# Kernel optimization log

Hardware: AMD Instinct MI355X
Metric: run time of the kernel (lower is better)

Reference implementation:

```python
import jax, jax.numpy as jnp
from jax import lax
import numpy as np

DT = 0.02
STEP_JITTER = 0.01
NUM_STEPS = 180
B, H, W, D = 2, 512, 512, 128


def setup_inputs() -> dict:
    key = jax.random.key(0)
    k1, k2, k3 = jax.random.split(key, 3)
    camera_rotation = jnp.tile(jnp.eye(3, dtype=jnp.float32)[None], (B, 1, 1))
    camera_position = jnp.array([[0.0, 0.0, -2.5], [0.3, 0.2, -2.5]], dtype=jnp.float32)
    focal = 300.0 * jnp.ones((B, 2), dtype=jnp.float32)
    principal_point = jnp.full((B, 2), 256.0, dtype=jnp.float32)
    xs = jnp.arange(W, dtype=jnp.float32)
    ys = jnp.arange(H, dtype=jnp.float32)
    gx, gy = jnp.meshgrid(xs, ys, indexing='xy')  # [H,W]
    pixel_coords = jnp.broadcast_to(jnp.stack([gx, gy], -1)[None], (B, H, W, 2))
    template = jax.random.uniform(k1, (B, 4, D, D, D), dtype=jnp.float32)  # RGB + alpha volume
    background = jax.random.uniform(k2, (B, 3, H, W), dtype=jnp.float32)
    return {
        'camera_rotation': camera_rotation, 'camera_position': camera_position,
        'focal': focal, 'principal_point': principal_point,
        'pixel_coords': pixel_coords, 'template': template, 'background': background,
    }


def _trilinear_one(vol, pos):
    # vol [C,D,D,D] indexed [c,z,y,x]; pos [H,W,3] = (x,y,z) in [-1,1]
    Dv = vol.shape[-1]
    g = jnp.clip((pos + 1.0) * 0.5 * (Dv - 1), 0.0, Dv - 1)
    gx, gy, gz = g[..., 0], g[..., 1], g[..., 2]
    x0 = jnp.floor(gx).astype(jnp.int32); x1 = jnp.minimum(x0 + 1, Dv - 1)
    y0 = jnp.floor(gy).astype(jnp.int32); y1 = jnp.minimum(y0 + 1, Dv - 1)
    z0 = jnp.floor(gz).astype(jnp.int32); z1 = jnp.minimum(z0 + 1, Dv - 1)
    wx = (gx - x0)[None]; wy = (gy - y0)[None]; wz = (gz - z0)[None]
    at = lambda z, y, x: vol[:, z, y, x]  # [C,H,W]
    c00 = at(z0, y0, x0) * (1 - wx) + at(z0, y0, x1) * wx
    c01 = at(z0, y1, x0) * (1 - wx) + at(z0, y1, x1) * wx
    c10 = at(z1, y0, x0) * (1 - wx) + at(z1, y0, x1) * wx
    c11 = at(z1, y1, x0) * (1 - wx) + at(z1, y1, x1) * wx
    c0 = c00 * (1 - wy) + c01 * wy
    c1 = c10 * (1 - wy) + c11 * wy
    return c0 * (1 - wz) + c1 * wz  # [C,H,W]


def _march(camera_rotation, camera_position, focal, principal_point, pixel_coords, template, background):
    key = jax.random.key(42)
    rd = (pixel_coords - principal_point[:, None, None, :]) / focal[:, None, None, :]
    rd = jnp.concatenate([rd, jnp.ones_like(rd[..., :1])], axis=-1)
    # torch: sum(R[:,None,None,:,:] * d[...,:,None], dim=-2) == R^T @ d
    rd = jnp.einsum('bjk,bhwj->bhwk', camera_rotation, rd)
    rd = rd / jnp.sqrt(jnp.sum(rd * rd, axis=-1, keepdims=True))
    cp = camera_position[:, None, None, :]
    # ray/box intersection (no_grad in original)
    t1 = (-1.0 - cp) / rd
    t2 = (1.0 - cp) / rd
    t_min = jnp.maximum(jnp.minimum(t1[..., 0], t2[..., 0]),
                        jnp.maximum(jnp.minimum(t1[..., 1], t2[..., 1]),
                                    jnp.minimum(t1[..., 2], t2[..., 2])))
    t_max = jnp.minimum(jnp.maximum(t1[..., 0], t2[..., 0]),
                        jnp.minimum(jnp.maximum(t1[..., 1], t2[..., 1]),
                                    jnp.maximum(t1[..., 2], t2[..., 2])))
    hit = t_min < t_max
    t = jnp.maximum(jnp.where(hit, t_min, 0.0), 0.0)
    t = lax.stop_gradient(t)
    t = t - DT * jax.random.uniform(jax.random.fold_in(key, 0), t.shape, dtype=t.dtype)
    ray_pos = cp + rd * t[..., None]                      # [B,H,W,3]
    ray_rgb = jnp.zeros_like(jnp.moveaxis(ray_pos, -1, 1))  # [B,3,H,W]
    ray_alpha = jnp.zeros_like(ray_rgb[:, :1])             # [B,1,H,W]
    ray_length = jnp.zeros_like(ray_alpha)
    sample = jax.vmap(_trilinear_one)

    def body(carry, i):
        ray_pos, t, ray_rgb, ray_alpha, ray_length = carry
        valid = jnp.all((ray_pos > -1.0) & (ray_pos < 1.0), axis=-1)
        valid_f = valid[:, None].astype(ray_rgb.dtype)      # [B,1,H,W]
        s = sample(template, ray_pos)                       # [B,4,H,W]
        sample_rgb, sample_alpha = s[:, :3], s[:, 3:4]
        noise = jax.random.normal(jax.random.fold_in(key, i + 1), t.shape, dtype=t.dtype)
        step = lax.stop_gradient(DT * jnp.exp(STEP_JITTER * noise))  # [B,H,W]
        contrib = (jnp.minimum(ray_alpha + sample_alpha * step[:, None], 1.0) - ray_alpha) * valid_f
        ray_rgb = ray_rgb + sample_rgb * contrib
        ray_alpha = ray_alpha + contrib
        ray_length = ray_length + step[:, None] * (contrib == 0)
        ray_pos = ray_pos + rd * step[..., None]
        t = t + step
        return (ray_pos, t, ray_rgb, ray_alpha, ray_length), None

    carry = (ray_pos, t, ray_rgb, ray_alpha, ray_length)
    (ray_pos, t, ray_rgb, ray_alpha, ray_length), _ = lax.scan(body, carry, jnp.arange(NUM_STEPS))
    ray_length = ray_alpha * ray_length / (jnp.max(ray_length) + jnp.min(ray_length))
    ray_rgb = ray_rgb + (1.0 - ray_alpha) * jnp.maximum(background, 0.0)
    return ray_rgb, ray_alpha, ray_length


def reference(camera_rotation, camera_position, focal, principal_point, pixel_coords, template, background):
    return _march(camera_rotation, camera_position, focal, principal_point, pixel_coords, template, background)
```

## Files before the change

### kernel.cpp

```cpp
#include <hip/hip_runtime.h>
#include <stdint.h>

#pragma clang fp contract(off)

#define Bn 2
#define Hn 512
#define Wn 512
#define Dn 128
#define HW (Hn * Wn)
#define NRAY (Bn * HW)
#define NSTEP 180
#define DTC 0.02f
#define D3 (Dn * Dn * Dn)

#define WS_AOS_BYTE_OFF 4096
#define WS_AOS_BYTES ((size_t)Bn * D3 * 16)

typedef float f2 __attribute__((ext_vector_type(2)));

#define KEXP  ((float)(0.01 * (double)1.41421354f * 1.4426950408889634))
#define LOG2DT (-5.643856189774724f)

__device__ __forceinline__ uint32_t rotl32(uint32_t x, int n) {
    return (x << n) | (x >> (32 - n));
}

__device__ __forceinline__ void tf2x32(uint32_t k0, uint32_t k1,
                                       uint32_t& x0, uint32_t& x1) {
    uint32_t k2 = k0 ^ k1 ^ 0x1BD11BDAu;
    x0 += k0; x1 += k1;
    x0 += x1; x1 = rotl32(x1, 13); x1 ^= x0;
    x0 += x1; x1 = rotl32(x1, 15); x1 ^= x0;
    x0 += x1; x1 = rotl32(x1, 26); x1 ^= x0;
    x0 += x1; x1 = rotl32(x1, 6);  x1 ^= x0;
    x0 += k1; x1 += k2 + 1u;
    x0 += x1; x1 = rotl32(x1, 17); x1 ^= x0;
    x0 += x1; x1 = rotl32(x1, 29); x1 ^= x0;
    x0 += x1; x1 = rotl32(x1, 16); x1 ^= x0;
    x0 += x1; x1 = rotl32(x1, 24); x1 ^= x0;
    x0 += k2; x1 += k0 + 2u;
    x0 += x1; x1 = rotl32(x1, 13); x1 ^= x0;
    x0 += x1; x1 = rotl32(x1, 15); x1 ^= x0;
    x0 += x1; x1 = rotl32(x1, 26); x1 ^= x0;
    x0 += x1; x1 = rotl32(x1, 6);  x1 ^= x0;
    x0 += k0; x1 += k1 + 3u;
    x0 += x1; x1 = rotl32(x1, 17); x1 ^= x0;
    x0 += x1; x1 = rotl32(x1, 29); x1 ^= x0;
    x0 += x1; x1 = rotl32(x1, 16); x1 ^= x0;
    x0 += x1; x1 = rotl32(x1, 24); x1 ^= x0;
    x0 += k1; x1 += k2 + 4u;
    x0 += x1; x1 = rotl32(x1, 13); x1 ^= x0;
    x0 += x1; x1 = rotl32(x1, 15); x1 ^= x0;
    x0 += x1; x1 = rotl32(x1, 26); x1 ^= x0;
    x0 += x1; x1 = rotl32(x1, 6);  x1 ^= x0;
    x0 += k2; x1 += k0 + 5u;
}

__device__ __forceinline__ uint32_t pbits(uint32_t k0, uint32_t k1, uint32_t i) {
    uint32_t x0 = 0u, x1 = i;
    tf2x32(k0, k1, x0, x1);
    return x0 ^ x1;
}

__device__ __forceinline__ float erfinv_px(float x) {
    float a = x * x;
    float w = -__logf(1.0f - a);
    float p;
    if (w < 5.0f) {
        w = w - 2.5f;
        p = 2.81022636e-08f;
        p = fmaf(p, w, 3.43273939e-07f);
        p = fmaf(p, w, -3.5233877e-06f);
        p = fmaf(p, w, -4.39150654e-06f);
        p = fmaf(p, w, 0.00021858087f);
        p = fmaf(p, w, -0.00125372503f);
        p = fmaf(p, w, -0.00417768164f);
        p = fmaf(p, w, 0.246640727f);
        p = fmaf(p, w, 1.50140941f);
    } else {
        w = sqrtf(w) - 3.0f;
        p = -0.000200214257f;
        p = fmaf(p, w, 0.000100950558f);
        p = fmaf(p, w, 0.00134934322f);
        p = fmaf(p, w, -0.00367342844f);
        p = fmaf(p, w, 0.00573950773f);
        p = fmaf(p, w, -0.0076224613f);
        p = fmaf(p, w, 0.00943887047f);
        p = fmaf(p, w, 1.00167406f);
        p = fmaf(p, w, 2.83297682f);
    }
    return p * x;
}

__device__ __forceinline__ float step_from_bits(uint32_t bits) {
    float uf = __uint_as_float((bits >> 9) | 0x3f800000u);
    float uu = fmaxf(-0.99999994f, fmaf(uf, 2.0f, -3.0f));
    float pw = erfinv_px(uu);
    return __builtin_amdgcn_exp2f(fmaf(pw, KEXP, LOG2DT));
}

__device__ __forceinline__ f2 plerp(f2 a, f2 b, f2 wv) {
    return __builtin_elementwise_fma(wv, b - a, a);
}

__global__ void init_keys_kernel(uint32_t* __restrict__ ws) {
    int t = threadIdx.x;
    if (t <= 180) {
        uint32_t x0 = 0u, x1 = (uint32_t)t;
        tf2x32(0u, 42u, x0, x1);
        ws[2 * t]     = x0;
        ws[2 * t + 1] = x1;
    }
    if (t == 181) ws[362] = 0u;
    if (t == 182) ws[363] = 0x7f7fffffu;
}

__global__ __launch_bounds__(256) void repack_kernel(
    const float* __restrict__ tpl, float4* __restrict__ aos,
    uint32_t* __restrict__ ws) {
    if (blockIdx.x == 0) {
        int t = threadIdx.x;
        if (t <= 180) {
            uint32_t x0 = 0u, x1 = (uint32_t)t;
            tf2x32(0u, 42u, x0, x1);
            ws[2 * t]     = x0;
            ws[2 * t + 1] = x1;
        }
        if (t == 181) ws[362] = 0u;
        if (t == 182) ws[363] = 0x7f7fffffu;
    }
    int i = blockIdx.x * 256 + threadIdx.x;
    if (i >= Bn * D3) return;
    int b = i >> 21;
    int v = i & (D3 - 1);
    const float* base = tpl + (size_t)b * 4 * D3 + v;
    float4 o;
    o.x = base[0];
    o.y = base[D3];
    o.z = base[2 * D3];
    o.w = base[3 * D3];
    aos[i] = o;
}

template <bool PACKED>
__global__ __launch_bounds__(256) void march_kernel(
    const float* __restrict__ rot, const float* __restrict__ cpos,
    const float* __restrict__ focal, const float* __restrict__ pp,
    const float* __restrict__ pix, const float* __restrict__ tpl,
    const float4* __restrict__ aos,
    const float* __restrict__ bg, float* __restrict__ out,
    uint32_t* __restrict__ ws)
{
    #pragma clang fp contract(off)
    __shared__ uint2 skeys[181];
    for (int i = threadIdx.x; i < 181; i += 256) {
        skeys[i] = make_uint2(ws[2 * i], ws[2 * i + 1]);
    }
    __syncthreads();

    const int idx = blockIdx.x * 256 + threadIdx.x;
    const int b = idx >> 18;
    const int p = idx & (HW - 1);

    float px = pix[(size_t)idx * 2 + 0];
    float py = pix[(size_t)idx * 2 + 1];
    float v0 = (px - pp[b * 2 + 0]) / focal[b * 2 + 0];
    float v1 = (py - pp[b * 2 + 1]) / focal[b * 2 + 1];
    const float* R = rot + b * 9;
    float rdx = (R[0] * v0 + R[3] * v1) + R[6];
    float rdy = (R[1] * v0 + R[4] * v1) + R[7];
    float rdz = (R[2] * v0 + R[5] * v1) + R[8];
    float nrm = sqrtf((rdx * rdx + rdy * rdy) + rdz * rdz);
    rdx = rdx / nrm; rdy = rdy / nrm; rdz = rdz / nrm;
    float cpx = cpos[b * 3 + 0], cpy = cpos[b * 3 + 1], cpz = cpos[b * 3 + 2];

    float t1x = (-1.0f - cpx) / rdx, t2x = (1.0f - cpx) / rdx;
    float t1y = (-1.0f - cpy) / rdy, t2y = (1.0f - cpy) / rdy;
    float t1z = (-1.0f - cpz) / rdz, t2z = (1.0f - cpz) / rdz;
    float tmin = fmaxf(fminf(t1x, t2x), fmaxf(fminf(t1y, t2y), fminf(t1z, t2z)));
    float tmax = fminf(fmaxf(t1x, t2x), fminf(fmaxf(t1y, t2y), fmaxf(t1z, t2z)));
    bool hit = tmin < tmax;
    float t = fmaxf(hit ? tmin : 0.0f, 0.0f);

    {
        uint2 k0 = skeys[0];
        uint32_t bits = pbits(k0.x, k0.y, (uint32_t)idx);
        float u = __uint_as_float((bits >> 9) | 0x3f800000u) - 1.0f;
        u = fmaxf(0.0f, u);
        t = t - DTC * u;
    }

    float posx = cpx + rdx * t;
    float posy = cpy + rdy * t;
    float posz = cpz + rdz * t;

    float alpha = 0.0f, len = 0.0f;
    f2 acc_rg = {0.0f, 0.0f};
    float acc_b = 0.0f;
    const float* vol = tpl + (size_t)b * 4 * D3;
    const char* vbase = (const char*)(aos + (size_t)b * D3);
    bool entered = false;

    int i = 0;
    for (; i < NSTEP; ++i) {
        uint2 kk = skeys[i + 1];
        float step = step_from_bits(pbits(kk.x, kk.y, (uint32_t)idx));

        float m = fmaxf(fmaxf(fabsf(posx), fabsf(posy)), fabsf(posz));
        bool valid = m < 1.0f;
        bool sampling = fmaxf(m, alpha) < 1.0f;

        float contrib = 0.0f;
        if (sampling) {
            float gx = fmaf(posx, 63.5f, 63.5f);
            float gy = fmaf(posy, 63.5f, 63.5f);
            float gz = fmaf(posz, 63.5f, 63.5f);
            float fx = floorf(gx), fy = floorf(gy), fz = floorf(gz);
            float wx = gx - fx, wy = gy - fy, wz = gz - fz;
            int ix0 = (int)fx, iy0 = (int)fy, iz0 = (int)fz;

            float sx, sy, sz, sw;
            if (PACKED) {
                uint32_t xb  = (uint32_t)min(ix0, Dn - 2) << 4;
                float wxe = (ix0 < Dn - 1) ? wx : 1.0f;
                uint32_t yb0 = (uint32_t)iy0 << 11;
                uint32_t yb1 = min(yb0 + (1u << 11), (uint32_t)(Dn - 1) << 11);
                uint32_t zb0 = (uint32_t)iz0 << 18;
                uint32_t zb1 = min(zb0 + (1u << 18), (uint32_t)(Dn - 1) << 18);

                uint32_t o00 = zb0 + yb0 + xb;
                uint32_t o01 = zb0 + yb1 + xb;
                uint32_t o10 = zb1 + yb0 + xb;
                uint32_t o11 = zb1 + yb1 + xb;

                float4 A00 = *(const float4*)(vbase + o00);
                float4 B00 = *(const float4*)(vbase + o00 + 16);
                float4 A01 = *(const float4*)(vbase + o01);
                float4 B01 = *(const float4*)(vbase + o01 + 16);
                float4 A10 = *(const float4*)(vbase + o10);
                float4 B10 = *(const float4*)(vbase + o10 + 16);
                float4 A11 = *(const float4*)(vbase + o11);
                float4 B11 = *(const float4*)(vbase + o11 + 16);

                f2 wxv = {wxe, wxe}, wyv = {wy, wy}, wzv = {wz, wz};
                f2 c00rg = plerp((f2){A00.x, A00.y}, (f2){B00.x, B00.y}, wxv);
                f2 c00ba = plerp((f2){A00.z, A00.w}, (f2){B00.z, B00.w}, wxv);
                f2 c01rg = plerp((f2){A01.x, A01.y}, (f2){B01.x, B01.y}, wxv);
                f2 c01ba = plerp((f2){A01.z, A01.w}, (f2){B01.z, B01.w}, wxv);
                f2 c10rg = plerp((f2){A10.x, A10.y}, (f2){B10.x, B10.y}, wxv);
                f2 c10ba = plerp((f2){A10.z, A10.w}, (f2){B10.z, B10.w}, wxv);
                f2 c11rg = plerp((f2){A11.x, A11.y}, (f2){B11.x, B11.y}, wxv);
                f2 c11ba = plerp((f2){A11.z, A11.w}, (f2){B11.z, B11.w}, wxv);
                f2 c0rg = plerp(c00rg, c01rg, wyv);
                f2 c0ba = plerp(c00ba, c01ba, wyv);
                f2 c1rg = plerp(c10rg, c11rg, wyv);
                f2 c1ba = plerp(c10ba, c11ba, wyv);
                f2 srg = plerp(c0rg, c1rg, wzv);
                f2 sba = plerp(c0ba, c1ba, wzv);
                sx = srg.x; sy = srg.y; sz = sba.x; sw = sba.y;
            } else {
                int ix1 = min(ix0 + 1, Dn - 1);
                int iy1 = min(iy0 + 1, Dn - 1);
                int iz1 = min(iz0 + 1, Dn - 1);
                float owx = 1.0f - wx, owy = 1.0f - wy, owz = 1.0f - wz;
                size_t o00 = ((size_t)iz0 * Dn + iy0) * Dn;
                size_t o01 = ((size_t)iz0 * Dn + iy1) * Dn;
                size_t o10 = ((size_t)iz1 * Dn + iy0) * Dn;
                size_t o11 = ((size_t)iz1 * Dn + iy1) * Dn;
                float s[4];
                #pragma unroll
                for (int c = 0; c < 4; ++c) {
                    const float* vc = vol + (size_t)c * D3;
                    float c00 = vc[o00 + ix0] * owx + vc[o00 + ix1] * wx;
                    float c01 = vc[o01 + ix0] * owx + vc[o01 + ix1] * wx;
                    float c10 = vc[o10 + ix0] * owx + vc[o10 + ix1] * wx;
                    float c11 = vc[o11 + ix0] * owx + vc[o11 + ix1] * wx;
                    float cc0 = c00 * owy + c01 * wy;
                    float cc1 = c10 * owy + c11 * wy;
                    s[c] = cc0 * owz + cc1 * wz;
                }
                sx = s[0]; sy = s[1]; sz = s[2]; sw = s[3];
            }
            contrib = fminf(fmaf(sw, step, alpha), 1.0f) - alpha;
            f2 cv = {contrib, contrib};
            acc_rg = __builtin_elementwise_fma((f2){sx, sy}, cv, acc_rg);
            acc_b = fmaf(sz, contrib, acc_b);
        }
        alpha = alpha + contrib;
        if (contrib == 0.0f) len = len + step;
        posx = fmaf(rdx, step, posx);
        posy = fmaf(rdy, step, posy);
        posz = fmaf(rdz, step, posz);

        bool done = (alpha >= 1.0f) || (entered && !valid);
        entered = entered || valid;
        if (__all(done)) { ++i; break; }
    }
    for (; i < NSTEP; ++i) {
        uint2 kk = skeys[i + 1];
        len = len + step_from_bits(pbits(kk.x, kk.y, (uint32_t)idx));
    }

    size_t obase = (size_t)b * 3 * HW + p;
    out[obase]            = acc_rg.x + (1.0f - alpha) * fmaxf(bg[obase], 0.0f);
    out[obase + HW]       = acc_rg.y + (1.0f - alpha) * fmaxf(bg[obase + HW], 0.0f);
    out[obase + 2 * HW]   = acc_b   + (1.0f - alpha) * fmaxf(bg[obase + 2 * HW], 0.0f);
    out[(size_t)Bn * 3 * HW + (size_t)b * HW + p] = alpha;
    out[(size_t)Bn * 4 * HW + (size_t)b * HW + p] = len;

    __shared__ float smax[256];
    __shared__ float smin[256];
    smax[threadIdx.x] = len;
    smin[threadIdx.x] = len;
    __syncthreads();
    for (int s = 128; s > 0; s >>= 1) {
        if (threadIdx.x < s) {
            smax[threadIdx.x] = fmaxf(smax[threadIdx.x], smax[threadIdx.x + s]);
            smin[threadIdx.x] = fminf(smin[threadIdx.x], smin[threadIdx.x + s]);
        }
        __syncthreads();
    }
    if (threadIdx.x == 0) {
        atomicMax((unsigned int*)&ws[362], __float_as_uint(smax[0]));
        atomicMin((unsigned int*)&ws[363], __float_as_uint(smin[0]));
    }
}

__global__ void finalize_kernel(float* __restrict__ out,
                                const uint32_t* __restrict__ ws) {
    #pragma clang fp contract(off)
    int i = blockIdx.x * blockDim.x + threadIdx.x;
    if (i >= NRAY) return;
    float mx = __uint_as_float(ws[362]);
    float mn = __uint_as_float(ws[363]);
    float a = out[(size_t)Bn * 3 * HW + i];
    size_t loff = (size_t)Bn * 4 * HW + i;
    float l = out[loff];
    out[loff] = (a * l) / (mx + mn);
}

extern "C" void kernel_launch(void* const* d_in, const int* in_sizes, int n_in,
                              void* d_out, int out_size, void* d_ws, size_t ws_size,
                              hipStream_t stream) {
    const float* rot   = (const float*)d_in[0];
    const float* cpos  = (const float*)d_in[1];
    const float* focal = (const float*)d_in[2];
    const float* pp    = (const float*)d_in[3];
    const float* pix   = (const float*)d_in[4];
    const float* tpl   = (const float*)d_in[5];
    const float* bg    = (const float*)d_in[6];
    float* out = (float*)d_out;
    uint32_t* ws = (uint32_t*)d_ws;
    float4* aos = (float4*)((char*)d_ws + WS_AOS_BYTE_OFF);

    const bool packed = ws_size >= WS_AOS_BYTE_OFF + WS_AOS_BYTES;

    if (packed) {
        hipLaunchKernelGGL(repack_kernel, dim3((Bn * D3) / 256), dim3(256), 0,
                           stream, tpl, aos, ws);
        hipLaunchKernelGGL(march_kernel<true>, dim3(NRAY / 256), dim3(256), 0,
                           stream, rot, cpos, focal, pp, pix, tpl, aos, bg, out, ws);
    } else {
        hipLaunchKernelGGL(init_keys_kernel, dim3(1), dim3(256), 0, stream, ws);
        hipLaunchKernelGGL(march_kernel<false>, dim3(NRAY / 256), dim3(256), 0,
                           stream, rot, cpos, focal, pp, pix, tpl, aos, bg, out, ws);
    }
    hipLaunchKernelGGL(finalize_kernel, dim3(NRAY / 256), dim3(256), 0, stream,
                       out, ws);
}
```

Before: 434.7 us.

## Batch Threefry step generation four-wide and unroll march loop by four

Computes four steps' Threefry random bits together in interleaved form so the integer hash chains run side by side and expose instruction-level parallelism. The march loop is unrolled by four, checking wave-wide termination only every four steps. Waves whose rays all miss the volume skip straight to the length-only tail, and the tail also uses the four-wide generator. Launch bounds now request four blocks per SM, which caps registers and adds some redundant work from the coarser exit check.

```diff
diff --git a/kernel.cpp b/kernel.cpp
--- a/kernel.cpp
+++ b/kernel.cpp
@@ -63,6 +63,7 @@
 }
 
 __device__ __forceinline__ float erfinv_px(float x) {
+    #pragma clang fp contract(off)
     float a = x * x;
     float w = -__logf(1.0f - a);
     float p;
@@ -93,10 +94,43 @@
 }
 
 __device__ __forceinline__ float step_from_bits(uint32_t bits) {
+    #pragma clang fp contract(off)
     float uf = __uint_as_float((bits >> 9) | 0x3f800000u);
     float uu = fmaxf(-0.99999994f, fmaf(uf, 2.0f, -3.0f));
     float pw = erfinv_px(uu);
     return __builtin_amdgcn_exp2f(fmaf(pw, KEXP, LOG2DT));
+}
+
+__device__ __forceinline__ void steps4(uint2 kk0, uint2 kk1,
+                                       uint2 kk2, uint2 kk3,
+                                       uint32_t idx, float s[4]) {
+    uint32_t k0[4] = {kk0.x, kk1.x, kk2.x, kk3.x};
+    uint32_t k1[4] = {kk0.y, kk1.y, kk2.y, kk3.y};
+    uint32_t k2[4], x0[4], x1[4];
+    #pragma unroll
+    for (int c = 0; c < 4; ++c) {
+        k2[c] = k0[c] ^ k1[c] ^ 0x1BD11BDAu;
+        x0[c] = k0[c];
+        x1[c] = idx + k1[c];
+    }
+#define RND4(r) { _Pragma("unroll") for (int c = 0; c < 4; ++c) { \
+        x0[c] += x1[c]; x1[c] = rotl32(x1[c], r); x1[c] ^= x0[c]; } }
+#define INJ4(A, B, inc) { _Pragma("unroll") for (int c = 0; c < 4; ++c) { \
+        x0[c] += A[c]; x1[c] += B[c] + inc; } }
+    RND4(13) RND4(15) RND4(26) RND4(6)
+    INJ4(k1, k2, 1u)
+    RND4(17) RND4(29) RND4(16) RND4(24)
+    INJ4(k2, k0, 2u)
+    RND4(13) RND4(15) RND4(26) RND4(6)
+    INJ4(k0, k1, 3u)
+    RND4(17) RND4(29) RND4(16) RND4(24)
+    INJ4(k1, k2, 4u)
+    RND4(13) RND4(15) RND4(26) RND4(6)
+    INJ4(k2, k0, 5u)
+#undef RND4
+#undef INJ4
+    #pragma unroll
+    for (int c = 0; c < 4; ++c) s[c] = step_from_bits(x0[c] ^ x1[c]);
 }
 
 __device__ __forceinline__ f2 plerp(f2 a, f2 b, f2 wv) {
@@ -143,7 +177,7 @@
 }
 
 template <bool PACKED>
-__global__ __launch_bounds__(256) void march_kernel(
+__global__ __launch_bounds__(256, 4) void march_kernel(
     const float* __restrict__ rot, const float* __restrict__ cpos,
     const float* __restrict__ focal, const float* __restrict__ pp,
     const float* __restrict__ pix, const float* __restrict__ tpl,
@@ -197,104 +231,123 @@
     float alpha = 0.0f, len = 0.0f;
     f2 acc_rg = {0.0f, 0.0f};
     float acc_b = 0.0f;
-    const float* vol = tpl + (size_t)b * 4 * D3;
-    const char* vbase = (const char*)(aos + (size_t)b * D3);
     bool entered = false;
+    bool done = !hit;
 
     int i = 0;
-    for (; i < NSTEP; ++i) {
-        uint2 kk = skeys[i + 1];
-        float step = step_from_bits(pbits(kk.x, kk.y, (uint32_t)idx));
-
-        float m = fmaxf(fmaxf(fabsf(posx), fabsf(posy)), fabsf(posz));
-        bool valid = m < 1.0f;
-        bool sampling = fmaxf(m, alpha) < 1.0f;
-
-        float contrib = 0.0f;
-        if (sampling) {
-            float gx = fmaf(posx, 63.5f, 63.5f);
-            float gy = fmaf(posy, 63.5f, 63.5f);
-            float gz = fmaf(posz, 63.5f, 63.5f);
-            float fx = floorf(gx), fy = floorf(gy), fz = floorf(gz);
-            float wx = gx - fx, wy = gy - fy, wz = gz - fz;
-            int ix0 = (int)fx, iy0 = (int)fy, iz0 = (int)fz;
-
-            float sx, sy, sz, sw;
-            if (PACKED) {
-                uint32_t xb  = (uint32_t)min(ix0, Dn - 2) << 4;
-                float wxe = (ix0 < Dn - 1) ? wx : 1.0f;
-                uint32_t yb0 = (uint32_t)iy0 << 11;
-                uint32_t yb1 = min(yb0 + (1u << 11), (uint32_t)(Dn - 1) << 11);
-                uint32_t zb0 = (uint32_t)iz0 << 18;
-                uint32_t zb1 = min(zb0 + (1u << 18), (uint32_t)(Dn - 1) << 18);
-
-                uint32_t o00 = zb0 + yb0 + xb;
-                uint32_t o01 = zb0 + yb1 + xb;
-                uint32_t o10 = zb1 + yb0 + xb;
-                uint32_t o11 = zb1 + yb1 + xb;
-
-                float4 A00 = *(const float4*)(vbase + o00);
-                float4 B00 = *(const float4*)(vbase + o00 + 16);
-                float4 A01 = *(const float4*)(vbase + o01);
-                float4 B01 = *(const float4*)(vbase + o01 + 16);
-                float4 A10 = *(const float4*)(vbase + o10);
-                float4 B10 = *(const float4*)(vbase + o10 + 16);
-                float4 A11 = *(const float4*)(vbase + o11);
-                float4 B11 = *(const float4*)(vbase + o11 + 16);
-
-                f2 wxv = {wxe, wxe}, wyv = {wy, wy}, wzv = {wz, wz};
-                f2 c00rg = plerp((f2){A00.x, A00.y}, (f2){B00.x, B00.y}, wxv);
-                f2 c00ba = plerp((f2){A00.z, A00.w}, (f2){B00.z, B00.w}, wxv);
-                f2 c01rg = plerp((f2){A01.x, A01.y}, (f2){B01.x, B01.y}, wxv);
-                f2 c01ba = plerp((f2){A01.z, A01.w}, (f2){B01.z, B01.w}, wxv);
-                f2 c10rg = plerp((f2){A10.x, A10.y}, (f2){B10.x, B10.y}, wxv);
-                f2 c10ba = plerp((f2){A10.z, A10.w}, (f2){B10.z, B10.w}, wxv);
-                f2 c11rg = plerp((f2){A11.x, A11.y}, (f2){B11.x, B11.y}, wxv);
-                f2 c11ba = plerp((f2){A11.z, A11.w}, (f2){B11.z, B11.w}, wxv);
-                f2 c0rg = plerp(c00rg, c01rg, wyv);
-                f2 c0ba = plerp(c00ba, c01ba, wyv);
-                f2 c1rg = plerp(c10rg, c11rg, wyv);
-                f2 c1ba = plerp(c10ba, c11ba, wyv);
-                f2 srg = plerp(c0rg, c1rg, wzv);
-                f2 sba = plerp(c0ba, c1ba, wzv);
-                sx = srg.x; sy = srg.y; sz = sba.x; sw = sba.y;
-            } else {
-                int ix1 = min(ix0 + 1, Dn - 1);
-                int iy1 = min(iy0 + 1, Dn - 1);
-                int iz1 = min(iz0 + 1, Dn - 1);
-                float owx = 1.0f - wx, owy = 1.0f - wy, owz = 1.0f - wz;
-                size_t o00 = ((size_t)iz0 * Dn + iy0) * Dn;
-                size_t o01 = ((size_t)iz0 * Dn + iy1) * Dn;
-                size_t o10 = ((size_t)iz1 * Dn + iy0) * Dn;
-                size_t o11 = ((size_t)iz1 * Dn + iy1) * Dn;
-                float s[4];
-                #pragma unroll
-                for (int c = 0; c < 4; ++c) {
-                    const float* vc = vol + (size_t)c * D3;
-                    float c00 = vc[o00 + ix0] * owx + vc[o00 + ix1] * wx;
-                    float c01 = vc[o01 + ix0] * owx + vc[o01 + ix1] * wx;
-                    float c10 = vc[o10 + ix0] * owx + vc[o10 + ix1] * wx;
-                    float c11 = vc[o11 + ix0] * owx + vc[o11 + ix1] * wx;
-                    float cc0 = c00 * owy + c01 * wy;
-                    float cc1 = c10 * owy + c11 * wy;
-                    s[c] = cc0 * owz + cc1 * wz;
+    if (!__all(done)) {
+        const char* vbase = (const char*)(aos + (size_t)b * D3);
+        const float* vol = tpl + (size_t)b * 4 * D3;
+        while (i < NSTEP) {
+            float s4[4];
+            steps4(skeys[i + 1], skeys[i + 2], skeys[i + 3], skeys[i + 4],
+                   (uint32_t)idx, s4);
+            #pragma unroll
+            for (int j = 0; j < 4; ++j) {
+                float step = s4[j];
+                float m = fmaxf(fmaxf(fabsf(posx), fabsf(posy)), fabsf(posz));
+                bool valid = m < 1.0f;
+                bool sampling = fmaxf(m, alpha) < 1.0f;
+
+                float contrib = 0.0f;
+                if (sampling) {
+                    float gx = fmaf(posx, 63.5f, 63.5f);
+                    float gy = fmaf(posy, 63.5f, 63.5f);
+                    float gz = fmaf(posz, 63.5f, 63.5f);
+                    float fx = floorf(gx), fy = floorf(gy), fz = floorf(gz);
+                    float wx = gx - fx, wy = gy - fy, wz = gz - fz;
+                    int ix0 = (int)fx, iy0 = (int)fy, iz0 = (int)fz;
+
+                    float sx, sy, sz, sw;
+                    if (PACKED) {
+                        uint32_t xb  = (uint32_t)min(ix0, Dn - 2) << 4;
+                        float wxe = (ix0 < Dn - 1) ? wx : 1.0f;
+                        uint32_t yb0 = (uint32_t)iy0 << 11;
+                        uint32_t yb1 = min(yb0 + (1u << 11), (uint32_t)(Dn - 1) << 11);
+                        uint32_t zb0 = (uint32_t)iz0 << 18;
+                        uint32_t zb1 = min(zb0 + (1u << 18), (uint32_t)(Dn - 1) << 18);
+
+                        uint32_t o00 = zb0 + yb0 + xb;
+                        uint32_t o01 = zb0 + yb1 + xb;
+                        uint32_t o10 = zb1 + yb0 + xb;
+                        uint32_t o11 = zb1 + yb1 + xb;
+
+                        float4 A00 = *(const float4*)(vbase + o00);
+                        float4 B00 = *(const float4*)(vbase + o00 + 16);
+                        float4 A01 = *(const float4*)(vbase + o01);
+                        float4 B01 = *(const float4*)(vbase + o01 + 16);
+                        float4 A10 = *(const float4*)(vbase + o10);
+                        float4 B10 = *(const float4*)(vbase + o10 + 16);
+                        float4 A11 = *(const float4*)(vbase + o11);
+                        float4 B11 = *(const float4*)(vbase + o11 + 16);
+
+                        f2 wxv = {wxe, wxe}, wyv = {wy, wy}, wzv = {wz, wz};
+                        f2 c00rg = plerp((f2){A00.x, A00.y}, (f2){B00.x, B00.y}, wxv);
+                        f2 c00ba = plerp((f2){A00.z, A00.w}, (f2){B00.z, B00.w}, wxv);
+                        f2 c01rg = plerp((f2){A01.x, A01.y}, (f2){B01.x, B01.y}, wxv);
+                        f2 c01ba = plerp((f2){A01.z, A01.w}, (f2){B01.z, B01.w}, wxv);
+                        f2 c10rg = plerp((f2){A10.x, A10.y}, (f2){B10.x, B10.y}, wxv);
+                        f2 c10ba = plerp((f2){A10.z, A10.w}, (f2){B10.z, B10.w}, wxv);
+                        f2 c11rg = plerp((f2){A11.x, A11.y}, (f2){B11.x, B11.y}, wxv);
+                        f2 c11ba = plerp((f2){A11.z, A11.w}, (f2){B11.z, B11.w}, wxv);
+                        f2 c0rg = plerp(c00rg, c01rg, wyv);
+                        f2 c0ba = plerp(c00ba, c01ba, wyv);
+                        f2 c1rg = plerp(c10rg, c11rg, wyv);
+                        f2 c1ba = plerp(c10ba, c11ba, wyv);
+                        f2 srg = plerp(c0rg, c1rg, wzv);
+                        f2 sba = plerp(c0ba, c1ba, wzv);
+                        sx = srg.x; sy = srg.y; sz = sba.x; sw = sba.y;
+                    } else {
+                        int ix1 = min(ix0 + 1, Dn - 1);
+                        int iy1 = min(iy0 + 1, Dn - 1);
+                        int iz1 = min(iz0 + 1, Dn - 1);
+                        float owx = 1.0f - wx, owy = 1.0f - wy, owz = 1.0f - wz;
+                        size_t o00 = ((size_t)iz0 * Dn + iy0) * Dn;
+                        size_t o01 = ((size_t)iz0 * Dn + iy1) * Dn;
+                        size_t o10 = ((size_t)iz1 * Dn + iy0) * Dn;
+                        size_t o11 = ((size_t)iz1 * Dn + iy1) * Dn;
+                        float s[4];
+                        #pragma unroll
+                        for (int c = 0; c < 4; ++c) {
+                            const float* vc = vol + (size_t)c * D3;
+                            float c00 = vc[o00 + ix0] * owx + vc[o00 + ix1] * wx;
+                            float c01 = vc[o01 + ix0] * owx + vc[o01 + ix1] * wx;
+                            float c10 = vc[o10 + ix0] * owx + vc[o10 + ix1] * wx;
+                            float c11 = vc[o11 + ix0] * owx + vc[o11 + ix1] * wx;
+                            float cc0 = c00 * owy + c01 * wy;
+                            float cc1 = c10 * owy + c11 * wy;
+                            s[c] = cc0 * owz + cc1 * wz;
+                        }
+                        sx = s[0]; sy = s[1]; sz = s[2]; sw = s[3];
+                    }
+                    contrib = fminf(fmaf(sw, step, alpha), 1.0f) - alpha;
+                    f2 cv = {contrib, contrib};
+                    acc_rg = __builtin_elementwise_fma((f2){sx, sy}, cv, acc_rg);
+                    acc_b = fmaf(sz, contrib, acc_b);
                 }
-                sx = s[0]; sy = s[1]; sz = s[2]; sw = s[3];
+                alpha = alpha + contrib;
+                if (contrib == 0.0f) len = len + step;
+                posx = fmaf(rdx, step, posx);
+                posy = fmaf(rdy, step, posy);
+                posz = fmaf(rdz, step, posz);
+
+                bool done_now = (alpha >= 1.0f) || (entered && !valid);
+                entered = entered || valid;
+                done = done || done_now;
             }
-            contrib = fminf(fmaf(sw, step, alpha), 1.0f) - alpha;
-            f2 cv = {contrib, contrib};
-            acc_rg = __builtin_elementwise_fma((f2){sx, sy}, cv, acc_rg);
-            acc_b = fmaf(sz, contrib, acc_b);
+            i += 4;
+            if (__all(done)) break;
         }
-        alpha = alpha + contrib;
-        if (contrib == 0.0f) len = len + step;
-        posx = fmaf(rdx, step, posx);
-        posy = fmaf(rdy, step, posy);
-        posz = fmaf(rdz, step, posz);
-
-        bool done = (alpha >= 1.0f) || (entered && !valid);
-        entered = entered || valid;
-        if (__all(done)) { ++i; break; }
+    }
+
+    for (; i + 3 < NSTEP; i += 4) {
+        float s4[4];
+        steps4(skeys[i + 1], skeys[i + 2], skeys[i + 3], skeys[i + 4],
+               (uint32_t)idx, s4);
+        len = len + s4[0];
+        len = len + s4[1];
+        len = len + s4[2];
+        len = len + s4[3];
     }
     for (; i < NSTEP; ++i) {
         uint2 kk = skeys[i + 1];
```

After: 417.8 us. 3.9% less time.
